# Kernel optimization log

Hardware: AMD Instinct MI355X
Metric: run time of the kernel (lower is better)

Reference implementation:

```python
import jax, jax.numpy as jnp
import numpy as np

HEADS = 8
GROUP_SIZE = 256
DIM = 512
QK_DIM = 512
M_GLOBAL = 64


def setup_inputs() -> dict:
    key = jax.random.key(0)
    ks = jax.random.split(key, 9)
    B, N = 2, 16384
    normed_x = jax.random.normal(ks[0], (B, N, DIM), dtype=jnp.float32)
    # idx_last must be a per-batch permutation of [0, N): gather reorders tokens,
    # the final scatter puts them back.
    perm = jnp.stack([jax.random.permutation(jax.random.fold_in(ks[1], b), N) for b in range(B)])
    idx_last = perm[..., None].astype(jnp.int32)  # [B, N, 1]
    dq = QK_DIM // HEADS
    dv = DIM // HEADS
    k_global = jax.random.normal(ks[2], (HEADS, M_GLOBAL, dq), dtype=jnp.float32)
    v_global = jax.random.normal(ks[3], (HEADS, M_GLOBAL, dv), dtype=jnp.float32)
    s = 0.02
    Wq = jax.random.normal(ks[4], (DIM, QK_DIM), dtype=jnp.float32) * s
    Wk = jax.random.normal(ks[5], (DIM, QK_DIM), dtype=jnp.float32) * s
    Wv = jax.random.normal(ks[6], (DIM, DIM), dtype=jnp.float32) * s
    Wproj = jax.random.normal(ks[7], (DIM, DIM), dtype=jnp.float32) * s
    return {"normed_x": normed_x, "idx_last": idx_last, "k_global": k_global,
            "v_global": v_global, "Wq": Wq, "Wk": Wk, "Wv": Wv, "Wproj": Wproj}


def _iasa_forward(normed_x, idx_last, k_global, v_global, Wq, Wk, Wv, Wproj):
    B, N, dim = normed_x.shape
    H = HEADS
    gs = min(N, GROUP_SIZE)
    ng = -(-N // gs)
    pad_n = ng * gs - N
    q = normed_x @ Wq  # [B, N, qk]
    k = normed_x @ Wk  # [B, N, qk]
    v = normed_x @ Wv  # [B, N, dim]
    # gather-reorder tokens
    q = jnp.take_along_axis(q, jnp.broadcast_to(idx_last, q.shape), axis=1)
    k = jnp.take_along_axis(k, jnp.broadcast_to(idx_last, k.shape), axis=1)
    v = jnp.take_along_axis(v, jnp.broadcast_to(idx_last, v.shape), axis=1)
    # pad queries with flipped tail to [B, ng*gs, qk]
    pq = jnp.concatenate([q, q[:, N - pad_n:N][:, ::-1]], axis=1)
    # pad k/v with flipped last (pad_n+gs) tokens -> length (ng+1)*gs
    pk = jnp.concatenate([k, k[:, N - pad_n - gs:N][:, ::-1]], axis=1)
    pv = jnp.concatenate([v, v[:, N - pad_n - gs:N][:, ::-1]], axis=1)
    dq = pq.shape[-1] // H
    dv = dim // H
    # queries: [B, ng, H, gs, dq]
    qg = pq.reshape(B, ng, gs, H, dq).transpose(0, 1, 3, 2, 4)
    # overlapping windows of size 2*gs, stride gs (unfold equivalent)
    kgrp = pk.reshape(B, ng + 1, gs, H, dq)
    vgrp = pv.reshape(B, ng + 1, gs, H, dv)
    kwin = jnp.concatenate([kgrp[:, :-1], kgrp[:, 1:]], axis=2).transpose(0, 1, 3, 2, 4)  # [B,ng,H,2gs,dq]
    vwin = jnp.concatenate([vgrp[:, :-1], vgrp[:, 1:]], axis=2).transpose(0, 1, 3, 2, 4)  # [B,ng,H,2gs,dv]
    scale = 1.0 / jnp.sqrt(jnp.asarray(dq, dtype=qg.dtype))
    # local attention
    s1 = jnp.einsum('bghqd,bghkd->bghqk', qg, kwin) * scale
    out1 = jnp.einsum('bghqk,bghkd->bghqd', jax.nn.softmax(s1, axis=-1), vwin)
    # global attention (k_global/v_global shared across batch and groups)
    s2 = jnp.einsum('bghqd,hmd->bghqm', qg, k_global) * scale
    out2 = jnp.einsum('bghqm,hmd->bghqd', jax.nn.softmax(s2, axis=-1), v_global)
    out = (out1 + out2).transpose(0, 1, 3, 2, 4).reshape(B, ng * gs, H * dv)[:, :N]
    # scatter back (inverse of the gather, since idx_last is a permutation)
    idxo = jnp.broadcast_to(idx_last, out.shape)
    bi = jnp.arange(B)[:, None, None]
    ci = jnp.arange(H * dv)[None, None, :]
    out = out.at[bi, idxo, ci].set(out)
    return out @ Wproj


def reference(normed_x, idx_last, k_global, v_global, Wq, Wk, Wv, Wproj):
    return _iasa_forward(normed_x, idx_last, k_global, v_global, Wq, Wk, Wv, Wproj)
```

## Files before the change

### kernel.cpp

```cpp
#include <hip/hip_runtime.h>
#include <hip/hip_bf16.h>

#define B_   2
#define N_   16384
#define H_   8
#define GS_  256
#define NG_  64

typedef unsigned short u16;
typedef __attribute__((ext_vector_type(8))) short bf16x8;
typedef __attribute__((ext_vector_type(4))) float f32x4;
typedef __attribute__((ext_vector_type(8))) unsigned short us8;
typedef __attribute__((ext_vector_type(4))) unsigned short us4;
typedef __attribute__((ext_vector_type(4))) unsigned int u32x4;
typedef __attribute__((ext_vector_type(2))) unsigned int u32x2;

__device__ __forceinline__ u16 f2b(float f){
  union { float f; unsigned u; } v; v.f = f;
  unsigned r = v.u + 0x7fffu + ((v.u >> 16) & 1u);
  return (u16)(r >> 16);
}

__device__ __forceinline__ u16 f2bh(float f){
  __hip_bfloat16 h = __float2bfloat16(f);
  u16 u; __builtin_memcpy(&u, &h, 2);
  return u;
}

__device__ __forceinline__ unsigned pk2(float a, float b){
  return ((unsigned)f2b(b) << 16) | (unsigned)f2b(a);
}

__device__ __forceinline__ void gload16(const void* g, const void* lds){
  __builtin_amdgcn_global_load_lds(
      (const __attribute__((address_space(1))) void*)g,
      (__attribute__((address_space(3))) void*)lds, 16, 0, 0);
}

__device__ __forceinline__ bf16x8 lds_read8(const u16* base, int row, int coloff){
  int byte = (row*128 + coloff) ^ ((row & 7) << 4);
  return *(const bf16x8*)((const char*)base + byte);
}

__device__ __forceinline__ void stout(float* p, float v){ *p = v; }
__device__ __forceinline__ void stout(u16* p, float v){ *p = f2b(v); }

__global__ void cvt_f32_bf16(const float4* __restrict__ in, us4* __restrict__ out, int n4){
  int i = blockIdx.x * 256 + threadIdx.x;
  if (i < n4){
    float4 v = in[i];
    us4 o;
    o[0] = f2b(v.x); o[1] = f2b(v.y); o[2] = f2b(v.z); o[3] = f2b(v.w);
    out[i] = o;
  }
}

__global__ void cvt_w_t(const float* __restrict__ W0, const float* __restrict__ W1,
                        const float* __restrict__ W2, const float* __restrict__ W3,
                        u16* __restrict__ T0, u16* __restrict__ T1,
                        u16* __restrict__ T2, u16* __restrict__ T3)
{
  int z = blockIdx.z;
  const float* W = (z==0)?W0:((z==1)?W1:((z==2)?W2:W3));
  u16* T = (z==0)?T0:((z==1)?T1:((z==2)?T2:T3));
  __shared__ float tile[16][17];
  int tx = threadIdx.x & 15, ty = threadIdx.x >> 4;
  int k0 = blockIdx.x*16, n0 = blockIdx.y*16;
  tile[ty][tx] = W[(k0+ty)*512 + n0 + tx];
  __syncthreads();
  T[(n0+ty)*512 + k0 + tx] = f2b(tile[tx][ty]);
}

template<typename OUT_T, bool MULTI, bool GATHA, bool SCATC>
__global__ __launch_bounds__(256, 2) void gemm_bf16k(
    const u16* __restrict__ A,
    const u16* __restrict__ Wt0, const u16* __restrict__ Wt1, const u16* __restrict__ Wt2,
    const int* __restrict__ perm,
    OUT_T* __restrict__ C, int ldc)
{
  __shared__ u16 Al[128*64];
  __shared__ u16 Bl[128*64];
  const int tid = threadIdx.x;
  const int l = tid & 63, w = tid >> 6;
  const int lr = l & 15, lg = l >> 4;
  const int bm = blockIdx.x, bn = blockIdx.y;
  const int wr = (w >> 1) * 64, wc = (w & 1) * 64;

  const u16* Wt; int ocolb; float qsc;
  if (MULTI){
    int wsel = bn >> 2;
    Wt = (wsel == 0) ? Wt0 : ((wsel == 1) ? Wt1 : Wt2);
    ocolb = (bn & 3) * 128;
    qsc = (wsel == 0) ? 0.18033688f : 1.0f;
  } else { Wt = Wt0; ocolb = bn * 128; qsc = 1.0f; }

  int arows[4];
#pragma unroll
  for (int i = 0; i < 4; ++i){
    int r = bm*128 + i*32 + (tid >> 3);
    arows[i] = GATHA ? ((r & ~(N_-1)) + perm[r]) : r;
  }

  f32x4 acc[4][4];
#pragma unroll
  for (int m = 0; m < 4; ++m)
#pragma unroll
    for (int n = 0; n < 4; ++n) acc[m][n] = (f32x4){0.f,0.f,0.f,0.f};

  const int c8 = tid & 7;
  for (int kk = 0; kk < 512; kk += 64){
#pragma unroll
    for (int i = 0; i < 4; ++i){
      int o = i*4096 + tid*16;
      int brow = o >> 7;
      gload16(A  + (size_t)arows[i]*512 + kk + c8*8, (const char*)Al + i*4096 + w*1024);
      gload16(Wt + (size_t)(ocolb + brow)*512 + kk + c8*8, (const char*)Bl + i*4096 + w*1024);
    }
    __syncthreads();
#pragma unroll
    for (int ks = 0; ks < 2; ++ks){
      bf16x8 af[4], bfv[4];
#pragma unroll
      for (int m = 0; m < 4; ++m) af[m]  = *(const bf16x8*)&Al[(wr + m*16 + lr)*64 + ks*32 + lg*8];
#pragma unroll
      for (int n = 0; n < 4; ++n) bfv[n] = *(const bf16x8*)&Bl[(wc + n*16 + lr)*64 + ks*32 + lg*8];
#pragma unroll
      for (int m = 0; m < 4; ++m)
#pragma unroll
        for (int n = 0; n < 4; ++n)
          acc[m][n] = __builtin_amdgcn_mfma_f32_16x16x32_bf16(af[m], bfv[n], acc[m][n], 0, 0, 0);
    }
    __syncthreads();
  }
#pragma unroll
  for (int m = 0; m < 4; ++m)
#pragma unroll
    for (int n = 0; n < 4; ++n)
#pragma unroll
      for (int j = 0; j < 4; ++j){
        int row = bm*128 + wr + m*16 + lg*4 + j;
        int col = bn*128 + wc + n*16 + lr;
        size_t orow = SCATC ? (size_t)((row & ~(N_-1)) + perm[row]) : (size_t)row;
        stout(&C[orow*ldc + col], acc[m][n][j] * qsc);
      }
}

#define COMPUTE_CHUNK(KBUF, VBUF, ACC, LAC) do { \
  f32x4 s_[4][4]; \
  _Pragma("unroll") \
  for (int n_ = 0; n_ < 4; ++n_){ _Pragma("unroll") for (int m_ = 0; m_ < 4; ++m_) s_[n_][m_] = (f32x4){0.f,0.f,0.f,0.f}; } \
  _Pragma("unroll") \
  for (int ks_ = 0; ks_ < 2; ++ks_){ \
    bf16x8 kf_[4]; \
    _Pragma("unroll") for (int n_ = 0; n_ < 4; ++n_) kf_[n_] = lds_read8((KBUF), n_*16 + lr, ks_*64 + lg*16); \
    _Pragma("unroll") for (int n_ = 0; n_ < 4; ++n_){ \
      _Pragma("unroll") for (int m_ = 0; m_ < 4; ++m_) \
        s_[n_][m_] = __builtin_amdgcn_mfma_f32_16x16x32_bf16(kf_[n_], qf[m_][ks_], s_[n_][m_], 0, 0, 0); } } \
  _Pragma("unroll") \
  for (int m_ = 0; m_ < 4; ++m_){ \
    float rs_ = 0.f; \
    _Pragma("unroll") for (int n_ = 0; n_ < 4; ++n_){ \
      _Pragma("unroll") for (int j_ = 0; j_ < 4; ++j_){ \
        float p_ = exp2f(s_[n_][m_][j_]); s_[n_][m_][j_] = p_; rs_ += p_; } } \
    (LAC)[m_] += rs_; } \
  _Pragma("unroll") \
  for (int mh_ = 0; mh_ < 2; ++mh_){ \
    _Pragma("unroll") for (int m2_ = 0; m2_ < 2; ++m2_){ \
      int m_ = mh_*2 + m2_; \
      int q_ = m2_*16 + lr; \
      _Pragma("unroll") for (int n_ = 0; n_ < 4; ++n_){ \
        u32x2 pk_; \
        pk_[0] = pk2(s_[n_][m_][0], s_[n_][m_][1]); \
        pk_[1] = pk2(s_[n_][m_][2], s_[n_][m_][3]); \
        int byte_ = (q_*128 + n_*32 + lg*8) ^ ((q_ & 7) << 4); \
        *(u32x2*)((char*)Pw + byte_) = pk_; } } \
    _Pragma("unroll") for (int ks_ = 0; ks_ < 2; ++ks_){ \
      bf16x8 pa_[2], vb_[4]; \
      _Pragma("unroll") for (int m2_ = 0; m2_ < 2; ++m2_) pa_[m2_] = lds_read8(Pw, m2_*16 + lr, ks_*64 + lg*16); \
      _Pragma("unroll") for (int n_ = 0; n_ < 4; ++n_) vb_[n_] = lds_read8((VBUF), n_*16 + lr, ks_*64 + lg*16); \
      _Pragma("unroll") for (int m2_ = 0; m2_ < 2; ++m2_){ \
        _Pragma("unroll") for (int n_ = 0; n_ < 4; ++n_) \
          (ACC)[mh_*2+m2_][n_] = __builtin_amdgcn_mfma_f32_16x16x32_bf16(pa_[m2_], vb_[n_], (ACC)[mh_*2+m2_][n_], 0, 0, 0); } } \
  } \
} while(0)

#define LOADKV(c) do { int c_ = (c); \
  if (c_ < 8){ \
    int p0k_ = g*GS_ + c_*64 + krow_; \
    int p1k_ = p0k_ + 32; \
    int rk0_ = (p0k_ < N_) ? p0k_ : (2*N_ - 1 - p0k_); \
    int rk1_ = (p1k_ < N_) ? p1k_ : (2*N_ - 1 - p1k_); \
    kr0 = *(const us8*)(qkv + (size_t)(b*N_ + rk0_)*1536 + 512 + h*64 + kc8_*8); \
    kr1 = *(const us8*)(qkv + (size_t)(b*N_ + rk1_)*1536 + 512 + h*64 + kc8_*8); \
    int p0v_ = g*GS_ + c_*64 + 2*pair; \
    int p1v_ = p0v_ + 1; \
    int rv0_ = (p0v_ < N_) ? p0v_ : (2*N_ - 1 - p0v_); \
    int rv1_ = (p1v_ < N_) ? p1v_ : (2*N_ - 1 - p1v_); \
    vr0 = *(const us8*)(qkv + (size_t)(b*N_ + rv0_)*1536 + 1024 + h*64 + dvb*8); \
    vr1 = *(const us8*)(qkv + (size_t)(b*N_ + rv1_)*1536 + 1024 + h*64 + dvb*8); \
  } else { \
    kr0 = *(const us8*)(kgb + (size_t)(h*64 + krow_)*64 + kc8_*8); \
    kr1 = *(const us8*)(kgb + (size_t)(h*64 + 32 + krow_)*64 + kc8_*8); \
    vr0 = *(const us8*)(vgb + (size_t)(h*64 + 2*pair)*64 + dvb*8); \
    vr1 = *(const us8*)(vgb + (size_t)(h*64 + 2*pair + 1)*64 + dvb*8); \
  } } while(0)

#define WRITEKV() do { \
  { int r0_ = krow_, r1_ = 32 + krow_; \
    *(us8*)((char*)Kb + ((r0_*128 + kc8_*16) ^ ((r0_ & 7) << 4))) = kr0; \
    *(us8*)((char*)Kb + ((r1_*128 + kc8_*16) ^ ((r1_ & 7) << 4))) = kr1; } \
  _Pragma("unroll") \
  for (int j_ = 0; j_ < 8; ++j_){ \
    int r_ = dvb*8 + j_; \
    int byte_ = (r_*128 + pair*4) ^ ((r_ & 7) << 4); \
    *(unsigned*)((char*)Vb + byte_) = (unsigned)vr0[j_] | ((unsigned)vr1[j_] << 16); } \
} while(0)

__global__ __launch_bounds__(256, 2) void attn_kernel(
    const u16* __restrict__ qkv,
    const u16* __restrict__ kgb,
    const u16* __restrict__ vgb,
    u16* __restrict__ outp)
{
  __shared__ u16 Pl[4][32*64];
  __shared__ u16 Kb[64*64];
  __shared__ u16 Vb[64*64];

  const int tid = threadIdx.x;
  const int l = tid & 63, w = tid >> 6;
  const int lr = l & 15, lg = l >> 4;
  const int pair = tid & 31, dvb = tid >> 5;
  const int krow_ = tid >> 3, kc8_ = tid & 7;

  const int g = blockIdx.x, h = blockIdx.y, b = blockIdx.z;

  bf16x8 qf[4][2];
#pragma unroll
  for (int m = 0; m < 4; ++m){
    int grow = g*GS_ + w*64 + m*16 + lr;
    const u16* qrow = qkv + (size_t)(b*N_ + grow)*1536 + h*64;
#pragma unroll
    for (int ks = 0; ks < 2; ++ks)
      qf[m][ks] = *(const bf16x8*)(qrow + ks*32 + lg*8);
  }

  u16* Pw = Pl[w];

  us8 kr0, kr1, vr0, vr1;
  LOADKV(0);
  WRITEKV();
  __syncthreads();

  f32x4 oacc[4][4];
  float lrun[4];
#pragma unroll
  for (int m = 0; m < 4; ++m)
#pragma unroll
    for (int n = 0; n < 4; ++n) oacc[m][n] = (f32x4){0.f,0.f,0.f,0.f};
#pragma unroll
  for (int m = 0; m < 4; ++m) lrun[m] = 0.f;

  for (int c = 0; c < 8; ++c){
    LOADKV(c + 1);
    COMPUTE_CHUNK(Kb, Vb, oacc, lrun);
    __syncthreads();
    WRITEKV();
    __syncthreads();
  }

  float i1[4];
#pragma unroll
  for (int m = 0; m < 4; ++m){
    float s1 = lrun[m];
    s1 += __shfl_xor(s1, 16); s1 += __shfl_xor(s1, 32);
    i1[m] = 1.f / s1;
  }
#pragma unroll
  for (int m = 0; m < 4; ++m)
#pragma unroll
    for (int j = 0; j < 4; ++j){
      float invb = __shfl(i1[m], lg*4 + j);
#pragma unroll
      for (int n = 0; n < 4; ++n) oacc[m][n][j] *= invb;
    }

  {
    f32x4 s_[4][4];
#pragma unroll
    for (int n_ = 0; n_ < 4; ++n_)
#pragma unroll
      for (int m_ = 0; m_ < 4; ++m_) s_[n_][m_] = (f32x4){0.f,0.f,0.f,0.f};
#pragma unroll
    for (int ks_ = 0; ks_ < 2; ++ks_){
      bf16x8 kf_[4];
#pragma unroll
      for (int n_ = 0; n_ < 4; ++n_) kf_[n_] = lds_read8(Kb, n_*16 + lr, ks_*64 + lg*16);
#pragma unroll
      for (int n_ = 0; n_ < 4; ++n_)
#pragma unroll
        for (int m_ = 0; m_ < 4; ++m_)
          s_[n_][m_] = __builtin_amdgcn_mfma_f32_16x16x32_bf16(kf_[n_], qf[m_][ks_], s_[n_][m_], 0, 0, 0);
    }
#pragma unroll
    for (int m_ = 0; m_ < 4; ++m_){
      float rs_ = 0.f;
#pragma unroll
      for (int n_ = 0; n_ < 4; ++n_)
#pragma unroll
        for (int j_ = 0; j_ < 4; ++j_){
          float p_ = exp2f(s_[n_][m_][j_]); s_[n_][m_][j_] = p_; rs_ += p_;
        }
      rs_ += __shfl_xor(rs_, 16); rs_ += __shfl_xor(rs_, 32);
      float iv_ = 1.f / rs_;
#pragma unroll
      for (int n_ = 0; n_ < 4; ++n_)
#pragma unroll
        for (int j_ = 0; j_ < 4; ++j_) s_[n_][m_][j_] *= iv_;
    }
#pragma unroll
    for (int mh_ = 0; mh_ < 2; ++mh_){
#pragma unroll
      for (int m2_ = 0; m2_ < 2; ++m2_){
        int m_ = mh_*2 + m2_;
        int q_ = m2_*16 + lr;
#pragma unroll
        for (int n_ = 0; n_ < 4; ++n_){
          u32x2 pk_;
          pk_[0] = pk2(s_[n_][m_][0], s_[n_][m_][1]);
          pk_[1] = pk2(s_[n_][m_][2], s_[n_][m_][3]);
          int byte_ = (q_*128 + n_*32 + lg*8) ^ ((q_ & 7) << 4);
          *(u32x2*)((char*)Pw + byte_) = pk_;
        }
      }
#pragma unroll
      for (int ks_ = 0; ks_ < 2; ++ks_){
        bf16x8 pa_[2], vb_[4];
#pragma unroll
        for (int m2_ = 0; m2_ < 2; ++m2_) pa_[m2_] = lds_read8(Pw, m2_*16 + lr, ks_*64 + lg*16);
#pragma unroll
        for (int n_ = 0; n_ < 4; ++n_) vb_[n_] = lds_read8(Vb, n_*16 + lr, ks_*64 + lg*16);
#pragma unroll
        for (int m2_ = 0; m2_ < 2; ++m2_)
#pragma unroll
          for (int n_ = 0; n_ < 4; ++n_)
            oacc[mh_*2+m2_][n_] = __builtin_amdgcn_mfma_f32_16x16x32_bf16(pa_[m2_], vb_[n_], oacc[mh_*2+m2_][n_], 0, 0, 0);
      }
    }
  }

#pragma unroll
  for (int mh = 0; mh < 2; ++mh){
#pragma unroll
    for (int m2 = 0; m2 < 2; ++m2)
#pragma unroll
      for (int n = 0; n < 4; ++n)
#pragma unroll
        for (int j = 0; j < 4; ++j){
          int row = m2*16 + lg*4 + j, col = n*16 + lr;
          int byte = (row*128 + col*2) ^ ((row & 7) << 4);
          *(u16*)((char*)Pw + byte) = f2bh(oacc[mh*2+m2][n][j]);
        }
    __builtin_amdgcn_s_waitcnt(0);
#pragma unroll
    for (int i4 = 0; i4 < 4; ++i4){
      int o = i4*1024 + l*16;
      int row = o >> 7, c8 = (o & 127) >> 4;
      int addr = o ^ ((row & 7) << 4);
      u32x4 d = *(const u32x4*)((const char*)Pw + addr);
      int orow = g*GS_ + w*64 + mh*32 + row;
      *(u32x4*)(outp + (size_t)(b*N_ + orow)*512 + h*64 + c8*8) = d;
    }
  }
}

extern "C" void kernel_launch(void* const* d_in, const int* in_sizes, int n_in,
                              void* d_out, int out_size, void* d_ws, size_t ws_size,
                              hipStream_t stream)
{
  const float* x  = (const float*)d_in[0];
  const int*  idx = (const int*)d_in[1];
  const float* kg = (const float*)d_in[2];
  const float* vg = (const float*)d_in[3];
  const float* Wq = (const float*)d_in[4];
  const float* Wk = (const float*)d_in[5];
  const float* Wv = (const float*)d_in[6];
  const float* Wp = (const float*)d_in[7];
  float* out = (float*)d_out;

  char* ws = (char*)d_ws;
  u16* Xb   = (u16*)ws;
  u16* qkv  = (u16*)(ws + 33554432);
  u16* Wqt  = (u16*)(ws + 134217728);
  u16* Wkt  = (u16*)(ws + 134217728 + 524288);
  u16* Wvt  = (u16*)(ws + 134217728 + 2*524288);
  u16* Wpt  = (u16*)(ws + 134217728 + 3*524288);
  u16* kgb  = (u16*)(ws + 134217728 + 4*524288);
  u16* vgb  = (u16*)(ws + 134217728 + 4*524288 + 65536);
  u16* attn_o = Xb;

  cvt_f32_bf16<<<16384, 256, 0, stream>>>((const float4*)x, (us4*)Xb, 16777216/4);
  cvt_f32_bf16<<<32, 256, 0, stream>>>((const float4*)kg, (us4*)kgb, 32768/4);
  cvt_f32_bf16<<<32, 256, 0, stream>>>((const float4*)vg, (us4*)vgb, 32768/4);
  cvt_w_t<<<dim3(32,32,4), 256, 0, stream>>>(Wq, Wk, Wv, Wp, Wqt, Wkt, Wvt, Wpt);
  gemm_bf16k<u16, true, true, false><<<dim3(256,12), 256, 0, stream>>>(Xb, Wqt, Wkt, Wvt, idx, qkv, 1536);
  attn_kernel<<<dim3(64,8,2), 256, 0, stream>>>(qkv, kgb, vgb, attn_o);
  gemm_bf16k<float, false, false, true><<<dim3(256,4), 256, 0, stream>>>(attn_o, Wpt, Wpt, Wpt, idx, out, 512);
}
```

Measured before the change: 213.8 us.

## Double-buffer K/V in LDS with direct global-to-LDS K loads

```diff
diff --git a/kernel.cpp b/kernel.cpp
--- a/kernel.cpp
+++ b/kernel.cpp
@@ -145,35 +145,71 @@
       }
 }
 
+#define ISSUEK(c, kbuf) do { int c_ = (c); \
+  _Pragma("unroll") for (int i_ = 0; i_ < 2; ++i_){ \
+    int row_ = i_*32 + (tid >> 3); \
+    int cc_ = ((tid & 7) ^ (row_ & 7)) * 8; \
+    const u16* src_; \
+    if (c_ < 8){ \
+      int p_ = g*GS_ + c_*64 + row_; \
+      int gi_ = (p_ < N_) ? p_ : (2*N_ - 1 - p_); \
+      src_ = qkv + (size_t)(b*N_ + gi_)*1536 + 512 + h*64 + cc_; \
+    } else { \
+      src_ = kgb + (size_t)(h*64 + row_)*64 + cc_; \
+    } \
+    gload16(src_, (const char*)(kbuf) + i_*4096 + w*1024); \
+  } } while(0)
+
+#define LOADV(c) do { int c_ = (c); \
+  if (c_ < 8){ \
+    int p0v_ = g*GS_ + c_*64 + 2*pair; \
+    int p1v_ = p0v_ + 1; \
+    int rv0_ = (p0v_ < N_) ? p0v_ : (2*N_ - 1 - p0v_); \
+    int rv1_ = (p1v_ < N_) ? p1v_ : (2*N_ - 1 - p1v_); \
+    vr0 = *(const us8*)(qkv + (size_t)(b*N_ + rv0_)*1536 + 1024 + h*64 + dvb*8); \
+    vr1 = *(const us8*)(qkv + (size_t)(b*N_ + rv1_)*1536 + 1024 + h*64 + dvb*8); \
+  } else { \
+    vr0 = *(const us8*)(vgb + (size_t)(h*64 + 2*pair)*64 + dvb*8); \
+    vr1 = *(const us8*)(vgb + (size_t)(h*64 + 2*pair + 1)*64 + dvb*8); \
+  } } while(0)
+
+#define WRITEV(vbuf) do { \
+  _Pragma("unroll") \
+  for (int j_ = 0; j_ < 8; ++j_){ \
+    int r_ = dvb*8 + j_; \
+    int byte_ = (r_*128 + pair*4) ^ ((r_ & 7) << 4); \
+    *(unsigned*)((char*)(vbuf) + byte_) = (unsigned)vr0[j_] | ((unsigned)vr1[j_] << 16); } \
+} while(0)
+
 #define COMPUTE_CHUNK(KBUF, VBUF, ACC, LAC) do { \
-  f32x4 s_[4][4]; \
-  _Pragma("unroll") \
-  for (int n_ = 0; n_ < 4; ++n_){ _Pragma("unroll") for (int m_ = 0; m_ < 4; ++m_) s_[n_][m_] = (f32x4){0.f,0.f,0.f,0.f}; } \
-  _Pragma("unroll") \
-  for (int ks_ = 0; ks_ < 2; ++ks_){ \
-    bf16x8 kf_[4]; \
-    _Pragma("unroll") for (int n_ = 0; n_ < 4; ++n_) kf_[n_] = lds_read8((KBUF), n_*16 + lr, ks_*64 + lg*16); \
-    _Pragma("unroll") for (int n_ = 0; n_ < 4; ++n_){ \
-      _Pragma("unroll") for (int m_ = 0; m_ < 4; ++m_) \
-        s_[n_][m_] = __builtin_amdgcn_mfma_f32_16x16x32_bf16(kf_[n_], qf[m_][ks_], s_[n_][m_], 0, 0, 0); } } \
-  _Pragma("unroll") \
-  for (int m_ = 0; m_ < 4; ++m_){ \
-    float rs_ = 0.f; \
-    _Pragma("unroll") for (int n_ = 0; n_ < 4; ++n_){ \
-      _Pragma("unroll") for (int j_ = 0; j_ < 4; ++j_){ \
-        float p_ = exp2f(s_[n_][m_][j_]); s_[n_][m_][j_] = p_; rs_ += p_; } } \
-    (LAC)[m_] += rs_; } \
   _Pragma("unroll") \
   for (int mh_ = 0; mh_ < 2; ++mh_){ \
-    _Pragma("unroll") for (int m2_ = 0; m2_ < 2; ++m2_){ \
-      int m_ = mh_*2 + m2_; \
-      int q_ = m2_*16 + lr; \
-      _Pragma("unroll") for (int n_ = 0; n_ < 4; ++n_){ \
-        u32x2 pk_; \
-        pk_[0] = pk2(s_[n_][m_][0], s_[n_][m_][1]); \
-        pk_[1] = pk2(s_[n_][m_][2], s_[n_][m_][3]); \
-        int byte_ = (q_*128 + n_*32 + lg*8) ^ ((q_ & 7) << 4); \
-        *(u32x2*)((char*)Pw + byte_) = pk_; } } \
+    _Pragma("unroll") \
+    for (int nh_ = 0; nh_ < 2; ++nh_){ \
+      f32x4 s_[2][2]; \
+      _Pragma("unroll") for (int n2_ = 0; n2_ < 2; ++n2_){ \
+        _Pragma("unroll") for (int m2_ = 0; m2_ < 2; ++m2_) s_[n2_][m2_] = (f32x4){0.f,0.f,0.f,0.f}; } \
+      _Pragma("unroll") for (int ks_ = 0; ks_ < 2; ++ks_){ \
+        bf16x8 kf_[2]; \
+        _Pragma("unroll") for (int n2_ = 0; n2_ < 2; ++n2_) \
+          kf_[n2_] = lds_read8((KBUF), (nh_*2+n2_)*16 + lr, ks_*64 + lg*16); \
+        _Pragma("unroll") for (int n2_ = 0; n2_ < 2; ++n2_){ \
+          _Pragma("unroll") for (int m2_ = 0; m2_ < 2; ++m2_) \
+            s_[n2_][m2_] = __builtin_amdgcn_mfma_f32_16x16x32_bf16(kf_[n2_], qf[mh_*2+m2_][ks_], s_[n2_][m2_], 0, 0, 0); } } \
+      _Pragma("unroll") for (int m2_ = 0; m2_ < 2; ++m2_){ \
+        float rs_ = 0.f; \
+        _Pragma("unroll") for (int n2_ = 0; n2_ < 2; ++n2_){ \
+          _Pragma("unroll") for (int j_ = 0; j_ < 4; ++j_){ \
+            float p_ = exp2f(s_[n2_][m2_][j_]); s_[n2_][m2_][j_] = p_; rs_ += p_; } } \
+        (LAC)[mh_*2+m2_] += rs_; \
+        int q_ = m2_*16 + lr; \
+        _Pragma("unroll") for (int n2_ = 0; n2_ < 2; ++n2_){ \
+          u32x2 pk_; \
+          pk_[0] = pk2(s_[n2_][m2_][0], s_[n2_][m2_][1]); \
+          pk_[1] = pk2(s_[n2_][m2_][2], s_[n2_][m2_][3]); \
+          int byte_ = (q_*128 + (nh_*2+n2_)*32 + lg*8) ^ ((q_ & 7) << 4); \
+          *(u32x2*)((char*)Pw + byte_) = pk_; } } \
+    } \
     _Pragma("unroll") for (int ks_ = 0; ks_ < 2; ++ks_){ \
       bf16x8 pa_[2], vb_[4]; \
       _Pragma("unroll") for (int m2_ = 0; m2_ < 2; ++m2_) pa_[m2_] = lds_read8(Pw, m2_*16 + lr, ks_*64 + lg*16); \
@@ -184,38 +220,6 @@
   } \
 } while(0)
 
-#define LOADKV(c) do { int c_ = (c); \
-  if (c_ < 8){ \
-    int p0k_ = g*GS_ + c_*64 + krow_; \
-    int p1k_ = p0k_ + 32; \
-    int rk0_ = (p0k_ < N_) ? p0k_ : (2*N_ - 1 - p0k_); \
-    int rk1_ = (p1k_ < N_) ? p1k_ : (2*N_ - 1 - p1k_); \
-    kr0 = *(const us8*)(qkv + (size_t)(b*N_ + rk0_)*1536 + 512 + h*64 + kc8_*8); \
-    kr1 = *(const us8*)(qkv + (size_t)(b*N_ + rk1_)*1536 + 512 + h*64 + kc8_*8); \
-    int p0v_ = g*GS_ + c_*64 + 2*pair; \
-    int p1v_ = p0v_ + 1; \
-    int rv0_ = (p0v_ < N_) ? p0v_ : (2*N_ - 1 - p0v_); \
-    int rv1_ = (p1v_ < N_) ? p1v_ : (2*N_ - 1 - p1v_); \
-    vr0 = *(const us8*)(qkv + (size_t)(b*N_ + rv0_)*1536 + 1024 + h*64 + dvb*8); \
-    vr1 = *(const us8*)(qkv + (size_t)(b*N_ + rv1_)*1536 + 1024 + h*64 + dvb*8); \
-  } else { \
-    kr0 = *(const us8*)(kgb + (size_t)(h*64 + krow_)*64 + kc8_*8); \
-    kr1 = *(const us8*)(kgb + (size_t)(h*64 + 32 + krow_)*64 + kc8_*8); \
-    vr0 = *(const us8*)(vgb + (size_t)(h*64 + 2*pair)*64 + dvb*8); \
-    vr1 = *(const us8*)(vgb + (size_t)(h*64 + 2*pair + 1)*64 + dvb*8); \
-  } } while(0)
-
-#define WRITEKV() do { \
-  { int r0_ = krow_, r1_ = 32 + krow_; \
-    *(us8*)((char*)Kb + ((r0_*128 + kc8_*16) ^ ((r0_ & 7) << 4))) = kr0; \
-    *(us8*)((char*)Kb + ((r1_*128 + kc8_*16) ^ ((r1_ & 7) << 4))) = kr1; } \
-  _Pragma("unroll") \
-  for (int j_ = 0; j_ < 8; ++j_){ \
-    int r_ = dvb*8 + j_; \
-    int byte_ = (r_*128 + pair*4) ^ ((r_ & 7) << 4); \
-    *(unsigned*)((char*)Vb + byte_) = (unsigned)vr0[j_] | ((unsigned)vr1[j_] << 16); } \
-} while(0)
-
 __global__ __launch_bounds__(256, 2) void attn_kernel(
     const u16* __restrict__ qkv,
     const u16* __restrict__ kgb,
@@ -223,14 +227,13 @@
     u16* __restrict__ outp)
 {
   __shared__ u16 Pl[4][32*64];
-  __shared__ u16 Kb[64*64];
-  __shared__ u16 Vb[64*64];
+  __shared__ u16 Kl[2][64*64];
+  __shared__ u16 Vl[2][64*64];
 
   const int tid = threadIdx.x;
   const int l = tid & 63, w = tid >> 6;
   const int lr = l & 15, lg = l >> 4;
   const int pair = tid & 31, dvb = tid >> 5;
-  const int krow_ = tid >> 3, kc8_ = tid & 7;
 
   const int g = blockIdx.x, h = blockIdx.y, b = blockIdx.z;
 
@@ -246,10 +249,13 @@
 
   u16* Pw = Pl[w];
 
-  us8 kr0, kr1, vr0, vr1;
-  LOADKV(0);
-  WRITEKV();
+  us8 vr0, vr1;
+  ISSUEK(0, Kl[0]);
+  LOADV(0);
+  WRITEV(Vl[0]);
   __syncthreads();
+  LOADV(1);
+  ISSUEK(1, Kl[1]);
 
   f32x4 oacc[4][4];
   float lrun[4];
@@ -261,11 +267,11 @@
   for (int m = 0; m < 4; ++m) lrun[m] = 0.f;
 
   for (int c = 0; c < 8; ++c){
-    LOADKV(c + 1);
-    COMPUTE_CHUNK(Kb, Vb, oacc, lrun);
+    int cur = c & 1;
+    COMPUTE_CHUNK(Kl[cur], Vl[cur], oacc, lrun);
+    WRITEV(Vl[cur ^ 1]);
     __syncthreads();
-    WRITEKV();
-    __syncthreads();
+    if (c < 7){ LOADV(c + 2); ISSUEK(c + 2, Kl[cur]); }
   }
 
   float i1[4];
@@ -294,7 +300,7 @@
     for (int ks_ = 0; ks_ < 2; ++ks_){
       bf16x8 kf_[4];
 #pragma unroll
-      for (int n_ = 0; n_ < 4; ++n_) kf_[n_] = lds_read8(Kb, n_*16 + lr, ks_*64 + lg*16);
+      for (int n_ = 0; n_ < 4; ++n_) kf_[n_] = lds_read8(Kl[0], n_*16 + lr, ks_*64 + lg*16);
 #pragma unroll
       for (int n_ = 0; n_ < 4; ++n_)
 #pragma unroll
@@ -338,7 +344,7 @@
 #pragma unroll
         for (int m2_ = 0; m2_ < 2; ++m2_) pa_[m2_] = lds_read8(Pw, m2_*16 + lr, ks_*64 + lg*16);
 #pragma unroll
-        for (int n_ = 0; n_ < 4; ++n_) vb_[n_] = lds_read8(Vb, n_*16 + lr, ks_*64 + lg*16);
+        for (int n_ = 0; n_ < 4; ++n_) vb_[n_] = lds_read8(Vl[0], n_*16 + lr, ks_*64 + lg*16);
 #pragma unroll
         for (int m2_ = 0; m2_ < 2; ++m2_)
 #pragma unroll
```

New measurement: 237.6 us. 11.1% more time.
